# Kernel tuning notes

Hardware: AMD Instinct MI355X
Metric: run time of the kernel (lower is better)

## Reference

```python
import jax, jax.numpy as jnp
import numpy as np

N_HEADS = 16
D_MODEL = 1024
D_K = D_MODEL // N_HEADS
B, S = 2, 2048


def setup_inputs() -> dict:
    key = jax.random.key(0)
    ks = jax.random.split(key, 12)
    sc = 1.0 / np.sqrt(D_MODEL)
    inp = {
        'query': jax.random.normal(ks[0], (B, S, D_MODEL), jnp.float32),
        'key':   jax.random.normal(ks[1], (B, S, D_MODEL), jnp.float32),
        'value': jax.random.normal(ks[2], (B, S, D_MODEL), jnp.float32),
        'mask':  jnp.ones((B, 1, 1, S), jnp.int32),
        'Wq': jax.random.normal(ks[3], (D_MODEL, D_MODEL), jnp.float32) * sc,
        'bq': jnp.zeros((D_MODEL,), jnp.float32),
        'Wk': jax.random.normal(ks[4], (D_MODEL, D_MODEL), jnp.float32) * sc,
        'bk': jnp.zeros((D_MODEL,), jnp.float32),
        'Wv': jax.random.normal(ks[5], (D_MODEL, D_MODEL), jnp.float32) * sc,
        'bv': jnp.zeros((D_MODEL,), jnp.float32),
        'Wo': jax.random.normal(ks[6], (D_MODEL, D_MODEL), jnp.float32) * sc,
        'bo': jnp.zeros((D_MODEL,), jnp.float32),
    }
    return inp


def reference(query, key, value, mask, Wq, bq, Wk, bk, Wv, bv, Wo, bo):
    # Linear projections (torch Linear: x @ W.T + b)
    q = query @ Wq.T + bq
    k = key @ Wk.T + bk
    v = value @ Wv.T + bv
    # [B, S, D] -> [B, H, S, d_k]
    def split_heads(x):
        b, s, _ = x.shape
        return x.reshape(b, s, N_HEADS, D_K).transpose(0, 2, 1, 3)
    q, k, v = split_heads(q), split_heads(k), split_heads(v)
    # scaled dot-product attention with explicit [B,H,S,S] scores
    att = jnp.einsum('bhqd,bhkd->bhqk', q, k) / jnp.sqrt(jnp.float32(D_K))
    att = jnp.where(mask == 0, -jnp.inf, att)
    scores = jax.nn.softmax(att, axis=-1)
    # dropout is identity in eval/reference mode
    out = jnp.einsum('bhqk,bhkd->bhqd', scores, v)
    b = out.shape[0]
    out = out.transpose(0, 2, 1, 3).reshape(b, -1, N_HEADS * D_K)
    return out @ Wo.T + bo
```

## Files before the change

kernel.cpp:

```cpp
#include <hip/hip_runtime.h>
#include <hip/hip_bf16.h>

#define DM   1024
#define SLEN 2048
#define NH   16
#define DK   64

typedef float f32x4 __attribute__((ext_vector_type(4)));
typedef short short8 __attribute__((ext_vector_type(8)));
typedef short short4v __attribute__((ext_vector_type(4)));

__device__ __forceinline__ unsigned short f2bf(float f) {
  union { float f; unsigned int u; } x; x.f = f;
  unsigned int r = x.u + 0x7fffu + ((x.u >> 16) & 1u);
  return (unsigned short)(r >> 16);
}

__device__ __forceinline__ void gload_lds16(const unsigned short* g, unsigned short* l) {
  __builtin_amdgcn_global_load_lds(
      (const __attribute__((address_space(1))) unsigned int*)g,
      (__attribute__((address_space(3))) unsigned int*)l, 16, 0, 0);
}

__device__ __forceinline__ f32x4 mfma32(short8 a, short8 b, f32x4 c) {
  return __builtin_amdgcn_mfma_f32_16x16x32_bf16(a, b, c, 0, 0, 0);
}

__device__ __forceinline__ f32x4 mfma16(short4v a, short4v b, f32x4 c) {
#if __has_builtin(__builtin_amdgcn_mfma_f32_16x16x16bf16_1k)
  return __builtin_amdgcn_mfma_f32_16x16x16bf16_1k(a, b, c, 0, 0, 0);
#else
  f32x4 d;
  asm volatile("v_mfma_f32_16x16x16_bf16 %0, %1, %2, %3"
               : "=v"(d) : "v"(a), "v"(b), "v"(c));
  return d;
#endif
}

struct ConvArgs { const float* src[7]; unsigned short* dst[7]; };

__global__ __launch_bounds__(256) void conv_kernel(ConvArgs a) {
  int blk = blockIdx.x, seg, base;
  if (blk < 6144) { seg = blk >> 11; base = blk & 2047; }
  else { int t = blk - 6144; seg = 3 + (t >> 9); base = t & 511; }
  const float* s = a.src[seg];
  unsigned short* d = a.dst[seg];
  int idx = (base * 256 + (int)threadIdx.x) * 8;
  float4 v0 = *(const float4*)(s + idx);
  float4 v1 = *(const float4*)(s + idx + 4);
  unsigned short o[8];
  o[0]=f2bf(v0.x); o[1]=f2bf(v0.y); o[2]=f2bf(v0.z); o[3]=f2bf(v0.w);
  o[4]=f2bf(v1.x); o[5]=f2bf(v1.y); o[6]=f2bf(v1.z); o[7]=f2bf(v1.w);
  *(uint4*)(d + idx) = *(uint4*)o;
}

template <int TN>
__device__ __forceinline__ void gemm_core(int mode,
                                          const unsigned short* __restrict__ A,
                                          const unsigned short* __restrict__ W,
                                          const float* __restrict__ bias,
                                          void* __restrict__ outp, float scale,
                                          int m0, int n0,
                                          unsigned short* As, unsigned short* Bs) {
  const int tid = threadIdx.x;
  const int lane = tid & 63;
  const int l15 = lane & 15;
  const int quad = lane >> 4;
  const int wv = tid >> 6;
  const int wm = (wv >> 1) * 64, wn = (wv & 1) * (TN / 2);
  const int NB = TN / 32;

  f32x4 acc[4][NB];
#pragma unroll
  for (int i = 0; i < 4; ++i)
#pragma unroll
    for (int j = 0; j < NB; ++j) acc[i][j] = (f32x4){0.f, 0.f, 0.f, 0.f};

  for (int k0 = 0; k0 < DM; k0 += 64) {
    __syncthreads();
#pragma unroll
    for (int i = 0; i < 4; ++i) {
      int c = tid + i * 256;
      int row = c >> 3, sc = ((c & 7) ^ (row & 7)) << 3;
      gload_lds16(A + (size_t)(m0 + row) * DM + k0 + sc, As + c * 8);
    }
#pragma unroll
    for (int i = 0; i < NB; ++i) {
      int c = tid + i * 256;
      int row = c >> 3, sc = ((c & 7) ^ (row & 7)) << 3;
      gload_lds16(W + (size_t)(n0 + row) * DM + k0 + sc, Bs + c * 8);
    }
    __syncthreads();
    short8 af[4][2], bf[NB][2];
#pragma unroll
    for (int i = 0; i < 4; ++i) {
      int r = wm + i * 16 + l15;
#pragma unroll
      for (int kf = 0; kf < 2; ++kf)
        af[i][kf] = *(const short8*)(As + r * 64 + (((kf * 4 + quad) ^ (r & 7)) << 3));
    }
#pragma unroll
    for (int j = 0; j < NB; ++j) {
      int r = wn + j * 16 + l15;
#pragma unroll
      for (int kf = 0; kf < 2; ++kf)
        bf[j][kf] = *(const short8*)(Bs + r * 64 + (((kf * 4 + quad) ^ (r & 7)) << 3));
    }
#pragma unroll
    for (int kf = 0; kf < 2; ++kf)
#pragma unroll
      for (int i = 0; i < 4; ++i)
#pragma unroll
        for (int j = 0; j < NB; ++j)
          acc[i][j] = mfma32(af[i][kf], bf[j][kf], acc[i][j]);
  }

#pragma unroll
  for (int i = 0; i < 4; ++i)
#pragma unroll
    for (int j = 0; j < NB; ++j) {
      int col = n0 + wn + j * 16 + l15;
      float bv = bias[col];
      int row0 = wm + i * 16 + (quad << 2) + m0;
      if (mode == 2) {
        unsigned short pk[4];
#pragma unroll
        for (int g = 0; g < 4; ++g) pk[g] = f2bf(acc[i][j][g] + bv);
        int d = col & (DK - 1), hh = col >> 6;
        int brow = row0 >> 11, srow = row0 & (SLEN - 1);
        size_t idx = ((size_t)((brow * NH + hh) * DK + d)) * SLEN + srow;
        *(uint2*)(((unsigned short*)outp) + idx) = *(uint2*)pk;
      } else if (mode == 0) {
#pragma unroll
        for (int g = 0; g < 4; ++g) {
          int row = row0 + g;
          float v = (acc[i][j][g] + bv) * scale;
          size_t idx = ((size_t)((row >> 11) * NH + (col >> 6))) * (SLEN * DK) +
                       (size_t)(row & (SLEN - 1)) * DK + (col & (DK - 1));
          ((unsigned short*)outp)[idx] = f2bf(v);
        }
      } else {
#pragma unroll
        for (int g = 0; g < 4; ++g)
          ((float*)outp)[(size_t)(row0 + g) * DM + col] = acc[i][j][g] + bv;
      }
    }
}

struct QKVArgs {
  const unsigned short* A[3];
  const unsigned short* W[3];
  const float* bias[3];
  unsigned short* out[3];
  float scale[3];
  int mode[3];
};

__global__ __launch_bounds__(256, 4) void gemm_qkv_kernel(QKVArgs a) {
  __shared__ unsigned short As[128 * 64], Bs[64 * 64];
  int z = blockIdx.z;
  gemm_core<64>(a.mode[z], a.A[z], a.W[z], a.bias[z], a.out[z], a.scale[z],
                blockIdx.x * 128, blockIdx.y * 64, As, Bs);
}

__global__ __launch_bounds__(256, 4) void gemm_o_kernel(const unsigned short* __restrict__ A,
                                                        const unsigned short* __restrict__ W,
                                                        const float* __restrict__ bias,
                                                        float* __restrict__ out) {
  __shared__ unsigned short As[128 * 64], Bs[64 * 64];
  gemm_core<64>(1, A, W, bias, out, 1.0f, blockIdx.x * 128, blockIdx.y * 64, As, Bs);
}

__global__ __launch_bounds__(512, 4) void attn_kernel(
    const unsigned short* __restrict__ Qw,
    const unsigned short* __restrict__ Kw,
    const unsigned short* __restrict__ Vtw,
    const int* __restrict__ mask,
    unsigned short* __restrict__ attn_out) {
  __shared__ uint4 smem4[4160];
  char* smb = (char*)smem4;
  float* Oex = (float*)smb;
  float* lsX = (float*)(smb + 33024);

  const int tid = threadIdx.x;
  const int lane = tid & 63;
  const int l15 = lane & 15;
  const int quad = lane >> 4;
  const int wv = tid >> 6;
  const int grp = wv >> 2;
  const int widx = wv & 3;
  const int tg = tid & 255;

  const int s0 = blockIdx.x * 128;
  const int bh = blockIdx.y;
  const int b = bh >> 4, h = bh & 15;
  const unsigned short* Qb = Qw + (size_t)bh * (SLEN * DK);
  const unsigned short* Kb = Kw + (size_t)bh * (SLEN * DK);
  const unsigned short* Vtb = Vtw + (size_t)bh * (SLEN * DK);

  const int qb = widx * 32;
  short8 bq[2][2];
#pragma unroll
  for (int qt = 0; qt < 2; ++qt)
#pragma unroll
    for (int kf = 0; kf < 2; ++kf)
      bq[qt][kf] = *(const short8*)(Qb + (size_t)(s0 + qb + qt * 16 + l15) * DK + kf * 32 + quad * 8);

  const int c0 = tg, c1 = tg + 256;
  const int r0c = c0 >> 3, s0c = ((c0 & 7) ^ (r0c & 7)) << 3;
  const int r1c = c1 >> 3, s1c = ((c1 & 7) ^ (r1c & 7)) << 3;

  {
    unsigned short* K0 = (unsigned short*)(smb + grp * 8192);
    unsigned short* V0 = (unsigned short*)(smb + 32768 + grp * 8192);
    int kv0 = grp * 64;
    gload_lds16(Kb + (size_t)(kv0 + r0c) * DK + s0c, K0 + c0 * 8);
    gload_lds16(Kb + (size_t)(kv0 + r1c) * DK + s1c, K0 + c1 * 8);
    gload_lds16(Vtb + (size_t)r0c * SLEN + kv0 + s0c, V0 + c0 * 8);
    gload_lds16(Vtb + (size_t)r1c * SLEN + kv0 + s1c, V0 + c1 * 8);
  }
  int mreg = 1;
  if (tg < 64) {
    ((float*)(smb + 65536 + grp * 256))[tg] = mask[b * SLEN + grp * 64 + tg] ? 0.0f : -1e30f;
    mreg = mask[b * SLEN + (2 + grp) * 64 + tg];
  }
  __syncthreads();

  f32x4 O[4][2];
#pragma unroll
  for (int dt = 0; dt < 4; ++dt)
#pragma unroll
    for (int qt = 0; qt < 2; ++qt) O[dt][qt] = (f32x4){0.f, 0.f, 0.f, 0.f};
  float lsum[2] = {0.f, 0.f};

  int cb = 0;
  for (int it = 0; it < 16; ++it) {
    const int nb = cb ^ 1;
    if (it < 15) {
      unsigned short* Kn = (unsigned short*)(smb + grp * 8192 + nb * 16384);
      unsigned short* Vn = (unsigned short*)(smb + 32768 + grp * 8192 + nb * 16384);
      int kvn = ((it + 1) * 2 + grp) * 64;
      gload_lds16(Kb + (size_t)(kvn + r0c) * DK + s0c, Kn + c0 * 8);
      gload_lds16(Kb + (size_t)(kvn + r1c) * DK + s1c, Kn + c1 * 8);
      gload_lds16(Vtb + (size_t)r0c * SLEN + kvn + s0c, Vn + c0 * 8);
      gload_lds16(Vtb + (size_t)r1c * SLEN + kvn + s1c, Vn + c1 * 8);
      if (tg < 64) {
        ((float*)(smb + 65536 + nb * 512 + grp * 256))[tg] = mreg ? 0.0f : -1e30f;
        if (it < 14) mreg = mask[b * SLEN + ((it + 2) * 2 + grp) * 64 + tg];
      }
    }

    unsigned short* KstG = (unsigned short*)(smb + grp * 8192 + cb * 16384);
    unsigned short* VstG = (unsigned short*)(smb + 32768 + grp * 8192 + cb * 16384);
    float* maskG = (float*)(smb + 65536 + cb * 512 + grp * 256);

    f32x4 st[4][2];
#pragma unroll
    for (int ct = 0; ct < 4; ++ct) {
      int r = ct * 16 + l15;
      short8 ka0 = *(const short8*)(KstG + r * 64 + ((quad ^ (r & 7)) << 3));
      short8 ka1 = *(const short8*)(KstG + r * 64 + (((4 + quad) ^ (r & 7)) << 3));
#pragma unroll
      for (int qt = 0; qt < 2; ++qt) {
        f32x4 z = (f32x4){0.f, 0.f, 0.f, 0.f};
        z = mfma32(ka0, bq[qt][0], z);
        st[ct][qt] = mfma32(ka1, bq[qt][1], z);
      }
    }
    short4v pf[4][2];
#pragma unroll
    for (int ct = 0; ct < 4; ++ct) {
      f32x4 ma = *(const f32x4*)(maskG + ct * 16 + quad * 4);
#pragma unroll
      for (int qt = 0; qt < 2; ++qt) {
        float p0 = __builtin_exp2f(st[ct][qt][0] + ma[0]);
        float p1 = __builtin_exp2f(st[ct][qt][1] + ma[1]);
        float p2 = __builtin_exp2f(st[ct][qt][2] + ma[2]);
        float p3 = __builtin_exp2f(st[ct][qt][3] + ma[3]);
        lsum[qt] += (p0 + p1) + (p2 + p3);
        union { short4v s; __hip_bfloat162 h[2]; } u;
        u.h[0] = __float22bfloat162_rn(float2{p0, p1});
        u.h[1] = __float22bfloat162_rn(float2{p2, p3});
        pf[ct][qt] = u.s;
      }
    }
#pragma unroll
    for (int dt = 0; dt < 4; ++dt) {
      int rd = dt * 16 + l15;
      short4v vf[4];
#pragma unroll
      for (int ct = 0; ct < 4; ++ct) {
        int slot = (ct * 2 + (quad >> 1)) ^ (rd & 7);
        vf[ct] = *(const short4v*)(VstG + rd * 64 + slot * 8 + (quad & 1) * 4);
      }
#pragma unroll
      for (int qt = 0; qt < 2; ++qt)
#pragma unroll
        for (int ct = 0; ct < 4; ++ct)
          O[dt][qt] = mfma16(vf[ct], pf[ct][qt], O[dt][qt]);
    }
    __syncthreads();
    cb = nb;
  }

#pragma unroll
  for (int qt = 0; qt < 2; ++qt) {
    lsum[qt] += __shfl_xor(lsum[qt], 16);
    lsum[qt] += __shfl_xor(lsum[qt], 32);
  }
  if (grp == 1) {
#pragma unroll
    for (int dt = 0; dt < 4; ++dt)
#pragma unroll
      for (int qt = 0; qt < 2; ++qt) {
        int qg = qb + qt * 16 + l15;
#pragma unroll
        for (int i = 0; i < 4; ++i)
          Oex[(dt * 16 + quad * 4 + i) * 129 + qg] = O[dt][qt][i];
      }
    if (quad == 0) {
      lsX[qb + lane] = lsum[0];
      lsX[qb + 16 + lane] = lsum[1];
    }
  }
  __syncthreads();
  if (grp == 0) {
#pragma unroll
    for (int qt = 0; qt < 2; ++qt) {
      int qg = qb + qt * 16 + l15;
      float inv = 1.0f / (lsum[qt] + lsX[qg]);
      int srow = s0 + qg;
#pragma unroll
      for (int dt = 0; dt < 4; ++dt) {
        int d0 = dt * 16 + quad * 4;
        unsigned short pk[4];
#pragma unroll
        for (int i = 0; i < 4; ++i)
          pk[i] = f2bf((O[dt][qt][i] + Oex[(d0 + i) * 129 + qg]) * inv);
        *(uint2*)(attn_out + (size_t)(b * SLEN + srow) * DM + h * DK + d0) = *(uint2*)pk;
      }
    }
  }
}

extern "C" void kernel_launch(void* const* d_in, const int* in_sizes, int n_in,
                              void* d_out, int out_size, void* d_ws, size_t ws_size,
                              hipStream_t stream) {
  (void)in_sizes; (void)n_in; (void)out_size; (void)ws_size;
  const float* query = (const float*)d_in[0];
  const float* key_  = (const float*)d_in[1];
  const float* value = (const float*)d_in[2];
  const int*   mask  = (const int*)d_in[3];
  const float* Wq = (const float*)d_in[4];
  const float* bq = (const float*)d_in[5];
  const float* Wk = (const float*)d_in[6];
  const float* bk = (const float*)d_in[7];
  const float* Wv = (const float*)d_in[8];
  const float* bv = (const float*)d_in[9];
  const float* Wo = (const float*)d_in[10];
  const float* bo = (const float*)d_in[11];
  float* out = (float*)d_out;

  const size_t WSZ = 1048576, XSZ = 4194304;
  unsigned short* base = (unsigned short*)d_ws;
  unsigned short* Wqb = base;
  unsigned short* Wkb = base + WSZ;
  unsigned short* Wvb = base + 2 * WSZ;
  unsigned short* Wob = base + 3 * WSZ;
  unsigned short* Xqb = base + 4 * WSZ;
  unsigned short* Xkb = Xqb + XSZ;
  unsigned short* Xvb = Xqb + 2 * XSZ;
  unsigned short* Qw  = Xqb + 3 * XSZ;
  unsigned short* Kw  = Qw + XSZ;
  unsigned short* Vtw = Qw + 2 * XSZ;
  unsigned short* attnb = Qw + 3 * XSZ;

  ConvArgs ca;
  ca.src[0] = query; ca.src[1] = key_; ca.src[2] = value;
  ca.src[3] = Wq; ca.src[4] = Wk; ca.src[5] = Wv; ca.src[6] = Wo;
  ca.dst[0] = Xqb; ca.dst[1] = Xkb; ca.dst[2] = Xvb;
  ca.dst[3] = Wqb; ca.dst[4] = Wkb; ca.dst[5] = Wvb; ca.dst[6] = Wob;
  conv_kernel<<<8192, 256, 0, stream>>>(ca);

  QKVArgs qa;
  qa.A[0] = Xqb; qa.A[1] = Xkb; qa.A[2] = Xvb;
  qa.W[0] = Wqb; qa.W[1] = Wkb; qa.W[2] = Wvb;
  qa.bias[0] = bq; qa.bias[1] = bk; qa.bias[2] = bv;
  qa.out[0] = Qw; qa.out[1] = Kw; qa.out[2] = Vtw;
  qa.scale[0] = 0.18033688011112042f;
  qa.scale[1] = 1.0f; qa.scale[2] = 1.0f;
  qa.mode[0] = 0; qa.mode[1] = 0; qa.mode[2] = 2;
  gemm_qkv_kernel<<<dim3(32, 16, 3), 256, 0, stream>>>(qa);

  attn_kernel<<<dim3(16, 32), 512, 0, stream>>>(Qw, Kw, Vtw, mask, attnb);

  gemm_o_kernel<<<dim3(32, 16), 256, 0, stream>>>(attnb, Wob, bo, out);
}
```

Measured before the change: 249.9 us.

## Stage GEMM epilogues through LDS for coalesced stores and remap block order

GEMM epilogues now write results into shared memory first and then emit wide 16-byte coalesced stores for the Q/K head layout, the transposed V layout and the fp32 output, replacing scattered 2-byte and 4-byte writes. The shared buffer is enlarged to 24 KB so it can double as the staging area. Block indices for the GEMM and attention kernels are also remapped from a 1D grid so groups of 8 consecutive blocks share the same tiles, aiming at better L2 reuse. This adds extra barriers and LDS traffic in the epilogue.

```diff
diff --git a/kernel.cpp b/kernel.cpp
--- a/kernel.cpp
+++ b/kernel.cpp
@@ -54,27 +54,26 @@
   *(uint4*)(d + idx) = *(uint4*)o;
 }
 
-template <int TN>
 __device__ __forceinline__ void gemm_core(int mode,
                                           const unsigned short* __restrict__ A,
                                           const unsigned short* __restrict__ W,
                                           const float* __restrict__ bias,
                                           void* __restrict__ outp, float scale,
-                                          int m0, int n0,
-                                          unsigned short* As, unsigned short* Bs) {
+                                          int m0, int n0, char* smem) {
+  unsigned short* As = (unsigned short*)smem;
+  unsigned short* Bs = (unsigned short*)(smem + 16384);
   const int tid = threadIdx.x;
   const int lane = tid & 63;
   const int l15 = lane & 15;
   const int quad = lane >> 4;
   const int wv = tid >> 6;
-  const int wm = (wv >> 1) * 64, wn = (wv & 1) * (TN / 2);
-  const int NB = TN / 32;
-
-  f32x4 acc[4][NB];
+  const int wm = (wv >> 1) * 64, wn = (wv & 1) * 32;
+
+  f32x4 acc[4][2];
 #pragma unroll
   for (int i = 0; i < 4; ++i)
 #pragma unroll
-    for (int j = 0; j < NB; ++j) acc[i][j] = (f32x4){0.f, 0.f, 0.f, 0.f};
+    for (int j = 0; j < 2; ++j) acc[i][j] = (f32x4){0.f, 0.f, 0.f, 0.f};
 
   for (int k0 = 0; k0 < DM; k0 += 64) {
     __syncthreads();
@@ -85,13 +84,13 @@
       gload_lds16(A + (size_t)(m0 + row) * DM + k0 + sc, As + c * 8);
     }
 #pragma unroll
-    for (int i = 0; i < NB; ++i) {
+    for (int i = 0; i < 2; ++i) {
       int c = tid + i * 256;
       int row = c >> 3, sc = ((c & 7) ^ (row & 7)) << 3;
       gload_lds16(W + (size_t)(n0 + row) * DM + k0 + sc, Bs + c * 8);
     }
     __syncthreads();
-    short8 af[4][2], bf[NB][2];
+    short8 af[4][2], bf[2][2];
 #pragma unroll
     for (int i = 0; i < 4; ++i) {
       int r = wm + i * 16 + l15;
@@ -100,7 +99,7 @@
         af[i][kf] = *(const short8*)(As + r * 64 + (((kf * 4 + quad) ^ (r & 7)) << 3));
     }
 #pragma unroll
-    for (int j = 0; j < NB; ++j) {
+    for (int j = 0; j < 2; ++j) {
       int r = wn + j * 16 + l15;
 #pragma unroll
       for (int kf = 0; kf < 2; ++kf)
@@ -111,40 +110,84 @@
 #pragma unroll
       for (int i = 0; i < 4; ++i)
 #pragma unroll
-        for (int j = 0; j < NB; ++j)
+        for (int j = 0; j < 2; ++j)
           acc[i][j] = mfma32(af[i][kf], bf[j][kf], acc[i][j]);
   }
 
-#pragma unroll
-  for (int i = 0; i < 4; ++i)
-#pragma unroll
-    for (int j = 0; j < NB; ++j) {
-      int col = n0 + wn + j * 16 + l15;
-      float bv = bias[col];
-      int row0 = wm + i * 16 + (quad << 2) + m0;
-      if (mode == 2) {
-        unsigned short pk[4];
-#pragma unroll
-        for (int g = 0; g < 4; ++g) pk[g] = f2bf(acc[i][j][g] + bv);
-        int d = col & (DK - 1), hh = col >> 6;
-        int brow = row0 >> 11, srow = row0 & (SLEN - 1);
-        size_t idx = ((size_t)((brow * NH + hh) * DK + d)) * SLEN + srow;
-        *(uint2*)(((unsigned short*)outp) + idx) = *(uint2*)pk;
-      } else if (mode == 0) {
-#pragma unroll
-        for (int g = 0; g < 4; ++g) {
-          int row = row0 + g;
-          float v = (acc[i][j][g] + bv) * scale;
-          size_t idx = ((size_t)((row >> 11) * NH + (col >> 6))) * (SLEN * DK) +
-                       (size_t)(row & (SLEN - 1)) * DK + (col & (DK - 1));
-          ((unsigned short*)outp)[idx] = f2bf(v);
-        }
-      } else {
+  const int hh = n0 >> 6;
+  const int brow = m0 >> 11;
+  const int srow0 = m0 & (SLEN - 1);
+
+  if (mode == 0) {
+    __syncthreads();
+    unsigned short* Ls = (unsigned short*)smem;
+#pragma unroll
+    for (int i = 0; i < 4; ++i)
+#pragma unroll
+      for (int j = 0; j < 2; ++j) {
+        int dloc = wn + j * 16 + l15;
+        float bv = bias[n0 + dloc];
+        int sl = wm + i * 16 + quad * 4;
 #pragma unroll
         for (int g = 0; g < 4; ++g)
-          ((float*)outp)[(size_t)(row0 + g) * DM + col] = acc[i][j][g] + bv;
-      }
-    }
+          Ls[(sl + g) * 66 + dloc] = f2bf((acc[i][j][g] + bv) * scale);
+      }
+    __syncthreads();
+    unsigned short* gout = (unsigned short*)outp +
+        ((size_t)(brow * NH + hh) * SLEN + srow0) * DK;
+    int sl = tid >> 1, dch = (tid & 1) * 32;
+#pragma unroll
+    for (int k = 0; k < 4; ++k)
+      *(uint4*)(gout + (size_t)sl * DK + dch + k * 8) =
+          *(const uint4*)(Ls + sl * 66 + dch + k * 8);
+  } else if (mode == 2) {
+    __syncthreads();
+    unsigned short* Ls = (unsigned short*)smem;
+#pragma unroll
+    for (int i = 0; i < 4; ++i)
+#pragma unroll
+      for (int j = 0; j < 2; ++j) {
+        int dloc = wn + j * 16 + l15;
+        float bv = bias[n0 + dloc];
+        int sl = wm + i * 16 + quad * 4;
+#pragma unroll
+        for (int g = 0; g < 4; ++g)
+          Ls[dloc * 132 + sl + g] = f2bf(acc[i][j][g] + bv);
+      }
+    __syncthreads();
+    unsigned short* gout = (unsigned short*)outp +
+        (size_t)(brow * NH + hh) * DK * SLEN + srow0;
+    int dloc = tid >> 2, sch = (tid & 3) * 32;
+#pragma unroll
+    for (int k = 0; k < 4; ++k)
+      *(uint4*)(gout + (size_t)dloc * SLEN + sch + k * 8) =
+          *(const uint4*)(Ls + dloc * 132 + sch + k * 8);
+  } else {
+    float* Lf = (float*)smem;
+#pragma unroll
+    for (int hf = 0; hf < 2; ++hf) {
+      __syncthreads();
+      if ((wv >> 1) == hf) {
+#pragma unroll
+        for (int i = 0; i < 4; ++i)
+#pragma unroll
+          for (int j = 0; j < 2; ++j) {
+            int dloc = wn + j * 16 + l15;
+            float bv = bias[n0 + dloc];
+            int sl = i * 16 + quad * 4;
+#pragma unroll
+            for (int g = 0; g < 4; ++g)
+              Lf[(sl + g) * 68 + dloc] = acc[i][j][g] + bv;
+          }
+      }
+      __syncthreads();
+      int row = tid >> 2, cch = (tid & 3) * 16;
+      float* gout = (float*)outp + (size_t)(m0 + hf * 64 + row) * DM + n0 + cch;
+#pragma unroll
+      for (int k = 0; k < 4; ++k)
+        *(float4*)(gout + k * 4) = *(const float4*)(Lf + row * 68 + cch + k * 4);
+    }
+  }
 }
 
 struct QKVArgs {
@@ -157,18 +200,23 @@
 };
 
 __global__ __launch_bounds__(256, 4) void gemm_qkv_kernel(QKVArgs a) {
-  __shared__ unsigned short As[128 * 64], Bs[64 * 64];
-  int z = blockIdx.z;
-  gemm_core<64>(a.mode[z], a.A[z], a.W[z], a.bias[z], a.out[z], a.scale[z],
-                blockIdx.x * 128, blockIdx.y * 64, As, Bs);
+  __shared__ char smem[24576];
+  int z = blockIdx.z, bid = blockIdx.x;
+  int xm = (bid & 7) + ((bid >> 7) << 3);
+  int yn = (bid >> 3) & 15;
+  gemm_core(a.mode[z], a.A[z], a.W[z], a.bias[z], a.out[z], a.scale[z],
+            xm * 128, yn * 64, smem);
 }
 
 __global__ __launch_bounds__(256, 4) void gemm_o_kernel(const unsigned short* __restrict__ A,
                                                         const unsigned short* __restrict__ W,
                                                         const float* __restrict__ bias,
                                                         float* __restrict__ out) {
-  __shared__ unsigned short As[128 * 64], Bs[64 * 64];
-  gemm_core<64>(1, A, W, bias, out, 1.0f, blockIdx.x * 128, blockIdx.y * 64, As, Bs);
+  __shared__ char smem[24576];
+  int bid = blockIdx.x;
+  int xm = (bid & 7) + ((bid >> 7) << 3);
+  int yn = (bid >> 3) & 15;
+  gemm_core(1, A, W, bias, out, 1.0f, xm * 128, yn * 64, smem);
 }
 
 __global__ __launch_bounds__(512, 4) void attn_kernel(
@@ -191,8 +239,9 @@
   const int widx = wv & 3;
   const int tg = tid & 255;
 
-  const int s0 = blockIdx.x * 128;
-  const int bh = blockIdx.y;
+  const int bid = blockIdx.x;
+  const int bh = (bid & 7) + ((bid >> 7) << 3);
+  const int s0 = ((bid >> 3) & 15) * 128;
   const int b = bh >> 4, h = bh & 15;
   const unsigned short* Qb = Qw + (size_t)bh * (SLEN * DK);
   const unsigned short* Kb = Kw + (size_t)bh * (SLEN * DK);
@@ -390,9 +439,9 @@
   qa.scale[0] = 0.18033688011112042f;
   qa.scale[1] = 1.0f; qa.scale[2] = 1.0f;
   qa.mode[0] = 0; qa.mode[1] = 0; qa.mode[2] = 2;
-  gemm_qkv_kernel<<<dim3(32, 16, 3), 256, 0, stream>>>(qa);
-
-  attn_kernel<<<dim3(16, 32), 512, 0, stream>>>(Qw, Kw, Vtw, mask, attnb);
-
-  gemm_o_kernel<<<dim3(32, 16), 256, 0, stream>>>(attnb, Wob, bo, out);
-}
+  gemm_qkv_kernel<<<dim3(512, 1, 3), 256, 0, stream>>>(qa);
+
+  attn_kernel<<<dim3(512), 512, 0, stream>>>(Qw, Kw, Vtw, mask, attnb);
+
+  gemm_o_kernel<<<dim3(512), 256, 0, stream>>>(attnb, Wob, bo, out);
+}
```

Measured after the change: 250.6 us. Within noise of the previous version (+0.3%).
